# Kernel tuning notes

Hardware: AMD Instinct MI355X
Metric: run time of the kernel (lower is better)

Reference implementation:

```python
import jax, jax.numpy as jnp
import numpy as np

N_HEAD = 16

def setup_inputs() -> dict:
    key = jax.random.key(0)
    ks = jax.random.split(key, 5)
    B, S, C = 4, 2048, 1024
    x = jax.random.normal(ks[0], (B, S, C), dtype=jnp.float32)
    w_qkv = jax.random.normal(ks[1], (C, 3 * C), dtype=jnp.float32) * (1.0 / np.sqrt(C))
    b_qkv = jnp.zeros((3 * C,), dtype=jnp.float32)
    w_proj = jax.random.normal(ks[2], (C, C), dtype=jnp.float32) * (1.0 / np.sqrt(C))
    b_proj = jnp.zeros((C,), dtype=jnp.float32)
    return {"x": x, "w_qkv": w_qkv, "b_qkv": b_qkv, "w_proj": w_proj, "b_proj": b_proj}

def reference(x, w_qkv, b_qkv, w_proj, b_proj):
    B, S, C = x.shape
    H = N_HEAD
    D = C // H
    qkv = x @ w_qkv + b_qkv                       # [B,S,3C]
    q, k, v = jnp.split(qkv, 3, axis=-1)
    # [B,S,C] -> [B,H,S,D]
    q = q.reshape(B, S, H, D).transpose(0, 2, 1, 3)
    k = k.reshape(B, S, H, D).transpose(0, 2, 1, 3)
    v = v.reshape(B, S, H, D).transpose(0, 2, 1, 3)
    scores = jnp.einsum('bhqd,bhkd->bhqk', q, k) / jnp.sqrt(jnp.float32(D))
    causal = jnp.tril(jnp.ones((S, S), dtype=bool))
    scores = jnp.where(causal[None, None], scores, -jnp.inf)
    weights = jax.nn.softmax(scores, axis=-1)     # dropout p=0 -> identity
    out = jnp.einsum('bhqk,bhkd->bhqd', weights, v)
    out = out.transpose(0, 2, 1, 3).reshape(B, S, C)
    return out @ w_proj + b_proj
```

## Files before the change

### kernel.cpp

```cpp
#include <hip/hip_runtime.h>

#define SDIM 2048
#define CDIM 1024
#define BDIM 4
#define HDIM 16
#define DDIM 64

#define ATT_SCALE 0.18033688011112042f

typedef __attribute__((ext_vector_type(8))) short bf16x8;
typedef __attribute__((ext_vector_type(4))) short bf16x4;
typedef __attribute__((ext_vector_type(4))) float f32x4;
typedef unsigned short u16;

#define MFMA __builtin_amdgcn_mfma_f32_16x16x32_bf16
#define LDS_ORDER_FENCE() __asm__ __volatile__("" ::: "memory")

__device__ __forceinline__ u16 f2b(float f) {
    union { float f; unsigned u; } v; v.f = f;
    unsigned r = v.u + 0x7FFFu + ((v.u >> 16) & 1u);
    return (u16)(r >> 16);
}
__device__ __forceinline__ u16 f2b_trunc(float f) {
    union { float f; unsigned u; } v; v.f = f;
    return (u16)(v.u >> 16);
}

typedef const __attribute__((address_space(1))) unsigned int* gas_t;
typedef __attribute__((address_space(3))) unsigned int* las_t;
__device__ __forceinline__ void cp16(const void* g, void* l) {
    __builtin_amdgcn_global_load_lds((gas_t)g, (las_t)l, 16, 0, 0);
}

__device__ __forceinline__ float fast_exp2(float x) {
#if __has_builtin(__builtin_amdgcn_exp2f)
    return __builtin_amdgcn_exp2f(x);
#else
    return __exp2f(x);
#endif
}

__global__ __launch_bounds__(256) void prep(
    const float* __restrict__ x, const float* __restrict__ w_qkv,
    const float* __restrict__ w_proj,
    u16* __restrict__ Xb, u16* __restrict__ WqT, u16* __restrict__ WpT)
{
    __shared__ __align__(16) u16 t[64][72];
    const int bx = blockIdx.x;
    const int tid = threadIdx.x;

    if (bx < 4096) {
        int i = (bx * 256 + tid) * 8;
        float4 a = *reinterpret_cast<const float4*>(&x[i]);
        float4 b = *reinterpret_cast<const float4*>(&x[i + 4]);
        u16 u[8];
        u[0]=f2b(a.x); u[1]=f2b(a.y); u[2]=f2b(a.z); u[3]=f2b(a.w);
        u[4]=f2b(b.x); u[5]=f2b(b.y); u[6]=f2b(b.z); u[7]=f2b(b.w);
        *reinterpret_cast<uint4*>(&Xb[i]) = *reinterpret_cast<uint4*>(u);
        return;
    }

    const float* src; u16* dst; int N, n0, k0;
    if (bx < 4096 + 768) {
        int b2 = bx - 4096;
        src = w_qkv; dst = WqT; N = 3 * CDIM;
        n0 = (b2 % 48) * 64; k0 = (b2 / 48) * 64;
    } else {
        int b2 = bx - 4864;
        src = w_proj; dst = WpT; N = CDIM;
        n0 = (b2 % 16) * 64; k0 = (b2 / 16) * 64;
    }
    const int K = CDIM;
#pragma unroll
    for (int it = 0; it < 4; it++) {
        int c = tid + it * 256;
        int r = c >> 4, c4 = (c & 15) * 4;
        float4 f = *reinterpret_cast<const float4*>(&src[(size_t)(k0 + r) * N + n0 + c4]);
        t[c4 + 0][r] = f2b(f.x);
        t[c4 + 1][r] = f2b(f.y);
        t[c4 + 2][r] = f2b(f.z);
        t[c4 + 3][r] = f2b(f.w);
    }
    __syncthreads();
#pragma unroll
    for (int it = 0; it < 2; it++) {
        int c = tid + it * 256;
        int r = c >> 3, c8 = (c & 7) * 8;
        *reinterpret_cast<uint4*>(&dst[(size_t)(n0 + r) * K + k0 + c8]) =
            *reinterpret_cast<const uint4*>(&t[r][c8]);
    }
}

#define PHASE_TAIL()                                                          \
    LDS_ORDER_FENCE();                                                        \
    __builtin_amdgcn_s_barrier();                                             \
    __asm__ __volatile__("s_waitcnt lgkmcnt(0)" ::: "memory");                \
    __builtin_amdgcn_sched_barrier(0)

#define PHASE_END()                                                           \
    LDS_ORDER_FENCE();                                                        \
    __builtin_amdgcn_s_barrier()

__global__ __launch_bounds__(256, 2) void gemm_qkv(
    const u16* __restrict__ A, const u16* __restrict__ Bt,
    const float* __restrict__ bias,
    u16* __restrict__ Qb, u16* __restrict__ Kb, u16* __restrict__ Vtb)
{
    __shared__ __align__(16) u16 smem[3 * 8192 + 3 * 4096];
    u16* const AsAll = smem;
    u16* const BsAll = smem + 3 * 8192;

    const int tid = threadIdx.x, lane = tid & 63, wave = tid >> 6;
    const int wm = wave >> 1, wn = wave & 1;
    const int l16 = lane & 15, quad = lane >> 4;
    const int bid = blockIdx.x;
    const int w = (bid & 7) * 96 + (bid >> 3);
    const int bx = w % 24, by = w / 24;
    const int m0 = by * 256, n0 = bx * 128;
    const int K = CDIM;

    const int su = (tid & 7) ^ ((tid >> 3) & 7);
    const int sr = ((tid >> 3) << 1) | (su >> 2);
    const int sc = su & 3;

    const int uc8 = ((((l16 & 1) << 2) | quad) ^ (l16 >> 1)) * 8;
    const int faB = (wm * 64 + (l16 >> 1)) * 64 + uc8;
    const int fbB = (wn * 32 + (l16 >> 1)) * 64 + uc8;

#define STG_A(sb, k0, s)  cp16(&A [(size_t)(m0 + (s) * 64 + sr) * K + (k0) + sc * 8], \
                               &AsAll[(sb) * 8192 + ((s) * 256 + wave * 64) * 8])
#define STG_B(sb, k0, s)  cp16(&Bt[(size_t)(n0 + (s) * 64 + sr) * K + (k0) + sc * 8], \
                               &BsAll[(sb) * 4096 + ((s) * 256 + wave * 64) * 8])
#define FRA(i) (*reinterpret_cast<const bf16x8*>(&AsB[faB + (i) * 512]))
#define FRB(j) (*reinterpret_cast<const bf16x8*>(&BsB[fbB + (j) * 512]))

    f32x4 acc[8][4];
#pragma unroll
    for (int i = 0; i < 8; i++)
#pragma unroll
        for (int j = 0; j < 4; j++) acc[i][j] = (f32x4){0.f, 0.f, 0.f, 0.f};

    const int NT = K / 32;
    STG_A(0, 0, 0); STG_A(0, 0, 1); STG_A(0, 0, 2); STG_A(0, 0, 3);
    STG_B(0, 0, 0); STG_B(0, 0, 1);
    STG_A(1, 32, 0); STG_A(1, 32, 1); STG_A(1, 32, 2); STG_A(1, 32, 3);
    STG_B(1, 32, 0); STG_B(1, 32, 1);
    __asm__ __volatile__("s_waitcnt vmcnt(6)" ::: "memory");
    __builtin_amdgcn_s_barrier();
    LDS_ORDER_FENCE();

    for (int t = 0; t < NT; t++) {
        const int buf = t % 3, sbuf = (t + 2) % 3;
        const int kst = (t + 2) * 32;
        const bool st = (t + 2) < NT;
        const u16* AsB = &AsAll[buf * 8192];
        const u16* BsB = &BsAll[buf * 4096];

        bf16x8 b0, b1, b2, b3, a0, a1, a2, a3;

        b0 = FRB(0); b1 = FRB(1); b2 = FRB(2); b3 = FRB(3);
        a0 = FRA(0); a1 = FRA(1); a2 = FRA(2); a3 = FRA(3);
        if (st) { STG_A(sbuf, kst, 0); STG_A(sbuf, kst, 1); STG_A(sbuf, kst, 2); }
        PHASE_TAIL();
        __builtin_amdgcn_s_setprio(1);
        acc[0][0] = MFMA(a0, b0, acc[0][0], 0, 0, 0);
        acc[0][1] = MFMA(a0, b1, acc[0][1], 0, 0, 0);
        acc[0][2] = MFMA(a0, b2, acc[0][2], 0, 0, 0);
        acc[0][3] = MFMA(a0, b3, acc[0][3], 0, 0, 0);
        acc[1][0] = MFMA(a1, b0, acc[1][0], 0, 0, 0);
        acc[1][1] = MFMA(a1, b1, acc[1][1], 0, 0, 0);
        acc[1][2] = MFMA(a1, b2, acc[1][2], 0, 0, 0);
        acc[1][3] = MFMA(a1, b3, acc[1][3], 0, 0, 0);
        acc[2][0] = MFMA(a2, b0, acc[2][0], 0, 0, 0);
        acc[2][1] = MFMA(a2, b1, acc[2][1], 0, 0, 0);
        acc[2][2] = MFMA(a2, b2, acc[2][2], 0, 0, 0);
        acc[2][3] = MFMA(a2, b3, acc[2][3], 0, 0, 0);
        acc[3][0] = MFMA(a3, b0, acc[3][0], 0, 0, 0);
        acc[3][1] = MFMA(a3, b1, acc[3][1], 0, 0, 0);
        acc[3][2] = MFMA(a3, b2, acc[3][2], 0, 0, 0);
        acc[3][3] = MFMA(a3, b3, acc[3][3], 0, 0, 0);
        __builtin_amdgcn_s_setprio(0);
        PHASE_END();

        a0 = FRA(4); a1 = FRA(5); a2 = FRA(6); a3 = FRA(7);
        if (st) { STG_A(sbuf, kst, 3); STG_B(sbuf, kst, 0); STG_B(sbuf, kst, 1); }
        PHASE_TAIL();
        __builtin_amdgcn_s_setprio(1);
        acc[4][0] = MFMA(a0, b0, acc[4][0], 0, 0, 0);
        acc[4][1] = MFMA(a0, b1, acc[4][1], 0, 0, 0);
        acc[4][2] = MFMA(a0, b2, acc[4][2], 0, 0, 0);
        acc[4][3] = MFMA(a0, b3, acc[4][3], 0, 0, 0);
        acc[5][0] = MFMA(a1, b0, acc[5][0], 0, 0, 0);
        acc[5][1] = MFMA(a1, b1, acc[5][1], 0, 0, 0);
        acc[5][2] = MFMA(a1, b2, acc[5][2], 0, 0, 0);
        acc[5][3] = MFMA(a1, b3, acc[5][3], 0, 0, 0);
        acc[6][0] = MFMA(a2, b0, acc[6][0], 0, 0, 0);
        acc[6][1] = MFMA(a2, b1, acc[6][1], 0, 0, 0);
        acc[6][2] = MFMA(a2, b2, acc[6][2], 0, 0, 0);
        acc[6][3] = MFMA(a2, b3, acc[6][3], 0, 0, 0);
        acc[7][0] = MFMA(a3, b0, acc[7][0], 0, 0, 0);
        acc[7][1] = MFMA(a3, b1, acc[7][1], 0, 0, 0);
        acc[7][2] = MFMA(a3, b2, acc[7][2], 0, 0, 0);
        acc[7][3] = MFMA(a3, b3, acc[7][3], 0, 0, 0);
        __builtin_amdgcn_s_setprio(0);
        if (t < NT - 2) {
            __asm__ __volatile__("s_waitcnt vmcnt(6)" ::: "memory");
        } else if (t == NT - 2) {
            __asm__ __volatile__("s_waitcnt vmcnt(0)" ::: "memory");
        }
        PHASE_END();
    }
#undef STG_A
#undef STG_B
#undef FRA
#undef FRB

    const int mm0 = m0 + wm * 128;
    const int bidx = mm0 >> 11, s0 = mm0 & 2047;
    const int n_base = n0 + wn * 64;
    u16* eb = &smem[wave * (16 * 68)];
    const int erow = lane >> 2, ec = (lane & 3) * 16;

    if (n0 >= 2 * CDIM) {
        const int h = (n_base - 2 * CDIM) >> 6;
        const size_t gb = ((size_t)(bidx * HDIM + h)) * DDIM * SDIM;
#pragma unroll
        for (int ih = 0; ih < 2; ih++) {
#pragma unroll
            for (int j = 0; j < 4; j++) {
                float bvj = bias[n_base + j * 16 + l16];
                LDS_ORDER_FENCE();
#pragma unroll
                for (int i = 0; i < 4; i++)
#pragma unroll
                    for (int r = 0; r < 4; r++)
                        eb[l16 * 68 + i * 16 + quad * 4 + r] =
                            f2b(acc[ih * 4 + i][j][r] + bvj);
                LDS_ORDER_FENCE();
                union { bf16x4 hp[4]; uint4 u[2]; } pk;
                pk.hp[0] = *reinterpret_cast<const bf16x4*>(&eb[erow * 68 + ec]);
                pk.hp[1] = *reinterpret_cast<const bf16x4*>(&eb[erow * 68 + ec + 4]);
                pk.hp[2] = *reinterpret_cast<const bf16x4*>(&eb[erow * 68 + ec + 8]);
                pk.hp[3] = *reinterpret_cast<const bf16x4*>(&eb[erow * 68 + ec + 12]);
                u16* gp = &Vtb[gb + (size_t)(j * 16 + erow) * SDIM + s0 + ih * 64 + ec];
                *reinterpret_cast<uint4*>(gp)     = pk.u[0];
                *reinterpret_cast<uint4*>(gp + 8) = pk.u[1];
            }
        }
    } else {
        const bool isK = (n_base >= CDIM);
        u16* dst = isK ? Kb : Qb;
        const float scale = isK ? 1.0f : ATT_SCALE;
        const int hh = (n_base & 1023) >> 6;
        const size_t hb = ((size_t)(bidx * HDIM + hh)) * SDIM;
        float bvj[4];
#pragma unroll
        for (int j = 0; j < 4; j++) bvj[j] = bias[n_base + j * 16 + l16];
#pragma unroll
        for (int i = 0; i < 8; i++) {
            LDS_ORDER_FENCE();
#pragma unroll
            for (int j = 0; j < 4; j++)
#pragma unroll
                for (int r = 0; r < 4; r++)
                    eb[(quad * 4 + r) * 68 + j * 16 + l16] =
                        f2b((acc[i][j][r] + bvj[j]) * scale);
            LDS_ORDER_FENCE();
            union { bf16x4 hp[4]; uint4 u[2]; } pk;
            pk.hp[0] = *reinterpret_cast<const bf16x4*>(&eb[erow * 68 + ec]);
            pk.hp[1] = *reinterpret_cast<const bf16x4*>(&eb[erow * 68 + ec + 4]);
            pk.hp[2] = *reinterpret_cast<const bf16x4*>(&eb[erow * 68 + ec + 8]);
            pk.hp[3] = *reinterpret_cast<const bf16x4*>(&eb[erow * 68 + ec + 12]);
            const int s = s0 + i * 16 + erow;
            u16* gp = &dst[(hb + s) * DDIM + ec];
            *reinterpret_cast<uint4*>(gp)     = pk.u[0];
            *reinterpret_cast<uint4*>(gp + 8) = pk.u[1];
        }
    }
}

__global__ __launch_bounds__(512, 4) void attn(
    const u16* __restrict__ Qb, const u16* __restrict__ Kb,
    const u16* __restrict__ Vtb, u16* __restrict__ Ob)
{
    __shared__ __align__(16) u16 Ks[2][64 * 64];
    __shared__ __align__(16) u16 Vts[2][64 * 64];
    __shared__ __align__(16) u16 Ps[8][32 * 68];

    const int tid = threadIdx.x;
    const int lane = tid & 63, wave = tid >> 6;
    const int l16 = lane & 15, quad = lane >> 4;
    const int x = blockIdx.x;
    const int bh = (x & 7) * 8 + ((x >> 3) & 7);
    const int g8 = (x >> 6) & 3;
    const int qt = (x >> 8) ? g8 : (7 - g8);
    const int q0 = qt * 256;
    const int b = bh >> 4, h = bh & 15;
    const size_t base = (size_t)bh * (SDIM * DDIM);

    const int cl0 = wave * 64 + lane;
    const int sr0 = cl0 >> 3, scc = cl0 & 7;
    const int sg0 = scc ^ (sr0 & 7);

    const int qr0 = q0 + wave * 32 + l16;
    bf16x8 aq0 = *reinterpret_cast<const bf16x8*>(&Qb[base + (size_t)qr0 * DDIM + quad * 8]);
    bf16x8 aq1 = *reinterpret_cast<const bf16x8*>(&Qb[base + (size_t)qr0 * DDIM + 32 + quad * 8]);
    const int qr1 = qr0 + 16;
    bf16x8 aq2 = *reinterpret_cast<const bf16x8*>(&Qb[base + (size_t)qr1 * DDIM + quad * 8]);
    bf16x8 aq3 = *reinterpret_cast<const bf16x8*>(&Qb[base + (size_t)qr1 * DDIM + 32 + quad * 8]);

    u16* Pw = &Ps[wave][0];

    f32x4 O[2][4];
    f32x4 Osum[2];
#pragma unroll
    for (int g = 0; g < 2; g++) {
        Osum[g] = (f32x4){0.f, 0.f, 0.f, 0.f};
#pragma unroll
        for (int j = 0; j < 4; j++) O[g][j] = (f32x4){0.f, 0.f, 0.f, 0.f};
    }
    const short onev = (l16 == 0) ? (short)0x3F80 : (short)0;
    const bf16x8 bones = {onev, onev, onev, onev, onev, onev, onev, onev};

    const int nkb = (qt + 1) * 4;
    const int Arow = q0 + wave * 32;

    cp16(&Kb [base + (size_t)sr0 * DDIM + sg0 * 8], &Ks[0][wave * 512]);
    cp16(&Vtb[base + (size_t)sr0 * SDIM + sg0 * 8], &Vts[0][wave * 512]);

    for (int kbi = 0; kbi < nkb; kbi++) {
        const int cur = kbi & 1;
        const int kb = kbi * 64;
        __syncthreads();
        if (kbi + 1 < nkb) {
            const int kb2 = kb + 64;
            cp16(&Kb [base + (size_t)(kb2 + sr0) * DDIM + sg0 * 8], &Ks[1 - cur][wave * 512]);
            cp16(&Vtb[base + (size_t)sr0 * SDIM + kb2 + sg0 * 8], &Vts[1 - cur][wave * 512]);
        }
        if (kb > Arow + 31) continue;

        const u16* Kc = &Ks[cur][0];
        const u16* Vc = &Vts[cur][0];

        f32x4 sc0[4], sc1[4];
#pragma unroll
        for (int j = 0; j < 4; j++) {
            int kr = j * 16 + l16;
            bf16x8 bk0 = *reinterpret_cast<const bf16x8*>(&Kc[(kr * 8 + ( quad      ^ (kr & 7))) * 8]);
            bf16x8 bk1 = *reinterpret_cast<const bf16x8*>(&Kc[(kr * 8 + ((quad + 4) ^ (kr & 7))) * 8]);
            f32x4 s = (f32x4){0.f, 0.f, 0.f, 0.f};
            s = MFMA(aq0, bk0, s, 0, 0, 0);
            s = MFMA(aq1, bk1, s, 0, 0, 0);
            sc0[j] = s;
            s = (f32x4){0.f, 0.f, 0.f, 0.f};
            s = MFMA(aq2, bk0, s, 0, 0, 0);
            s = MFMA(aq3, bk1, s, 0, 0, 0);
            sc1[j] = s;
        }
        if (kb + 63 > Arow) {
            const int qrel0 = Arow - kb;
#pragma unroll
            for (int j = 0; j < 4; j++) {
                int kk = j * 16 + l16;
#pragma unroll
                for (int r = 0; r < 4; r++) {
                    sc0[j][r] = (kk <= qrel0 + quad * 4 + r)      ? sc0[j][r] : -1e30f;
                    sc1[j][r] = (kk <= qrel0 + 16 + quad * 4 + r) ? sc1[j][r] : -1e30f;
                }
            }
        }
#pragma unroll
        for (int j = 0; j < 4; j++)
#pragma unroll
            for (int r = 0; r < 4; r++) {
                Pw[(quad * 4 + r) * 68 + j * 16 + l16]        = f2b_trunc(fast_exp2(sc0[j][r]));
                Pw[(16 + quad * 4 + r) * 68 + j * 16 + l16]   = f2b_trunc(fast_exp2(sc1[j][r]));
            }
        LDS_ORDER_FENCE();
        union { bf16x4 hp[2]; bf16x8 f; } a0u, a1u, a2u, a3u;
        a0u.hp[0] = *reinterpret_cast<const bf16x4*>(&Pw[l16 * 68 + quad * 8]);
        a0u.hp[1] = *reinterpret_cast<const bf16x4*>(&Pw[l16 * 68 + quad * 8 + 4]);
        a1u.hp[0] = *reinterpret_cast<const bf16x4*>(&Pw[l16 * 68 + 32 + quad * 8]);
        a1u.hp[1] = *reinterpret_cast<const bf16x4*>(&Pw[l16 * 68 + 32 + quad * 8 + 4]);
        a2u.hp[0] = *reinterpret_cast<const bf16x4*>(&Pw[(16 + l16) * 68 + quad * 8]);
        a2u.hp[1] = *reinterpret_cast<const bf16x4*>(&Pw[(16 + l16) * 68 + quad * 8 + 4]);
        a3u.hp[0] = *reinterpret_cast<const bf16x4*>(&Pw[(16 + l16) * 68 + 32 + quad * 8]);
        a3u.hp[1] = *reinterpret_cast<const bf16x4*>(&Pw[(16 + l16) * 68 + 32 + quad * 8 + 4]);

#pragma unroll
        for (int j = 0; j < 4; j++) {
            int vr = j * 16 + l16;
            bf16x8 bv0 = *reinterpret_cast<const bf16x8*>(&Vc[(vr * 8 + ( quad      ^ (vr & 7))) * 8]);
            bf16x8 bv1 = *reinterpret_cast<const bf16x8*>(&Vc[(vr * 8 + ((quad + 4) ^ (vr & 7))) * 8]);
            O[0][j] = MFMA(a0u.f, bv0, O[0][j], 0, 0, 0);
            O[0][j] = MFMA(a1u.f, bv1, O[0][j], 0, 0, 0);
            O[1][j] = MFMA(a2u.f, bv0, O[1][j], 0, 0, 0);
            O[1][j] = MFMA(a3u.f, bv1, O[1][j], 0, 0, 0);
        }
        Osum[0] = MFMA(a0u.f, bones, Osum[0], 0, 0, 0);
        Osum[0] = MFMA(a1u.f, bones, Osum[0], 0, 0, 0);
        Osum[1] = MFMA(a2u.f, bones, Osum[1], 0, 0, 0);
        Osum[1] = MFMA(a3u.f, bones, Osum[1], 0, 0, 0);
    }

#pragma unroll
    for (int g = 0; g < 2; g++) {
#pragma unroll
        for (int r = 0; r < 4; r++) {
            float l = __shfl(Osum[g][r], (lane & 48));
            float inv = 1.0f / l;
            int s = q0 + wave * 32 + g * 16 + quad * 4 + r;
#pragma unroll
            for (int j = 0; j < 4; j++)
                Ob[((size_t)(b * SDIM + s)) * CDIM + h * 64 + j * 16 + l16] =
                    f2b(O[g][j][r] * inv);
        }
    }
}

__global__ __launch_bounds__(512, 2) void gemm_proj(
    const u16* __restrict__ A, const u16* __restrict__ Bt,
    const float* __restrict__ bias, float* __restrict__ out)
{
    __shared__ __align__(16) u16 smem[3 * 16384 + 3 * 8192];
    u16* const AsAll = smem;
    u16* const BsAll = smem + 3 * 16384;

    const int tid = threadIdx.x, lane = tid & 63, wave = tid >> 6;
    const int wm = wave >> 1, wn = wave & 1;
    const int l16 = lane & 15, quad = lane >> 4;
    const int bid = blockIdx.x;
    const int w = (bid & 7) * 32 + (bid >> 3);
    const int bx = w & 7, by = w >> 3;
    const int m0 = by * 256, n0 = bx * 128;
    const int K = CDIM, N = CDIM;

    const int l8 = lane & 7, lr = lane >> 3;
    const int sg = l8 ^ lr;
    const int arow = wave * 8 + lr;

#define STG_A(sb, k0, s)  cp16(&A [(size_t)(m0 + (s) * 64 + arow) * K + (k0) + sg * 8], \
                               &AsAll[(sb) * 16384 + ((s) * 512 + wave * 64) * 8])
#define STG_B(sb, k0, s)  cp16(&Bt[(size_t)(n0 + (s) * 64 + arow) * K + (k0) + sg * 8], \
                               &BsAll[(sb) * 8192 + ((s) * 512 + wave * 64) * 8])
#define FRA(i, kk) (*reinterpret_cast<const bf16x8*>(                                   \
        &AsB[((wm * 64 + (i) * 16 + l16) * 8 + (((kk) * 4 + quad) ^ (l16 & 7))) * 8]))
#define FRB(j, kk) (*reinterpret_cast<const bf16x8*>(                                   \
        &BsB[((wn * 64 + (j) * 16 + l16) * 8 + (((kk) * 4 + quad) ^ (l16 & 7))) * 8]))

    f32x4 acc[4][4];
#pragma unroll
    for (int i = 0; i < 4; i++)
#pragma unroll
        for (int j = 0; j < 4; j++) acc[i][j] = (f32x4){0.f, 0.f, 0.f, 0.f};

    const int NT = K / 64;
    STG_A(0, 0, 0); STG_A(0, 0, 1); STG_A(0, 0, 2); STG_A(0, 0, 3);
    STG_B(0, 0, 0); STG_B(0, 0, 1);
    STG_A(1, 64, 0); STG_A(1, 64, 1); STG_A(1, 64, 2); STG_A(1, 64, 3);
    STG_B(1, 64, 0); STG_B(1, 64, 1);
    __asm__ __volatile__("s_waitcnt vmcnt(6)" ::: "memory");
    __builtin_amdgcn_s_barrier();
    LDS_ORDER_FENCE();

    for (int t = 0; t < NT; t++) {
        const int buf = t % 3, sbuf = (t + 2) % 3;
        const int kst = (t + 2) * 64;
        const bool st = (t + 2) < NT;
        const u16* AsB = &AsAll[buf * 16384];
        const u16* BsB = &BsAll[buf * 8192];

        bf16x8 b0, b1, b2, b3, a0, a1;

        b0 = FRB(0, 0); b1 = FRB(1, 0); b2 = FRB(2, 0); b3 = FRB(3, 0);
        a0 = FRA(0, 0); a1 = FRA(1, 0);
        if (st) { STG_A(sbuf, kst, 0); STG_A(sbuf, kst, 1); }
        PHASE_TAIL();
        __builtin_amdgcn_s_setprio(1);
        acc[0][0] = MFMA(a0, b0, acc[0][0], 0, 0, 0);
        acc[0][1] = MFMA(a0, b1, acc[0][1], 0, 0, 0);
        acc[0][2] = MFMA(a0, b2, acc[0][2], 0, 0, 0);
        acc[0][3] = MFMA(a0, b3, acc[0][3], 0, 0, 0);
        acc[1][0] = MFMA(a1, b0, acc[1][0], 0, 0, 0);
        acc[1][1] = MFMA(a1, b1, acc[1][1], 0, 0, 0);
        acc[1][2] = MFMA(a1, b2, acc[1][2], 0, 0, 0);
        acc[1][3] = MFMA(a1, b3, acc[1][3], 0, 0, 0);
        __builtin_amdgcn_s_setprio(0);
        PHASE_END();

        a0 = FRA(2, 0); a1 = FRA(3, 0);
        if (st) { STG_A(sbuf, kst, 2); STG_A(sbuf, kst, 3); }
        PHASE_TAIL();
        __builtin_amdgcn_s_setprio(1);
        acc[2][0] = MFMA(a0, b0, acc[2][0], 0, 0, 0);
        acc[2][1] = MFMA(a0, b1, acc[2][1], 0, 0, 0);
        acc[2][2] = MFMA(a0, b2, acc[2][2], 0, 0, 0);
        acc[2][3] = MFMA(a0, b3, acc[2][3], 0, 0, 0);
        acc[3][0] = MFMA(a1, b0, acc[3][0], 0, 0, 0);
        acc[3][1] = MFMA(a1, b1, acc[3][1], 0, 0, 0);
        acc[3][2] = MFMA(a1, b2, acc[3][2], 0, 0, 0);
        acc[3][3] = MFMA(a1, b3, acc[3][3], 0, 0, 0);
        __builtin_amdgcn_s_setprio(0);
        PHASE_END();

        b0 = FRB(0, 1); b1 = FRB(1, 1); b2 = FRB(2, 1); b3 = FRB(3, 1);
        a0 = FRA(0, 1); a1 = FRA(1, 1);
        if (st) { STG_B(sbuf, kst, 0); STG_B(sbuf, kst, 1); }
        PHASE_TAIL();
        __builtin_amdgcn_s_setprio(1);
        acc[0][0] = MFMA(a0, b0, acc[0][0], 0, 0, 0);
        acc[0][1] = MFMA(a0, b1, acc[0][1], 0, 0, 0);
        acc[0][2] = MFMA(a0, b2, acc[0][2], 0, 0, 0);
        acc[0][3] = MFMA(a0, b3, acc[0][3], 0, 0, 0);
        acc[1][0] = MFMA(a1, b0, acc[1][0], 0, 0, 0);
        acc[1][1] = MFMA(a1, b1, acc[1][1], 0, 0, 0);
        acc[1][2] = MFMA(a1, b2, acc[1][2], 0, 0, 0);
        acc[1][3] = MFMA(a1, b3, acc[1][3], 0, 0, 0);
        __builtin_amdgcn_s_setprio(0);
        PHASE_END();

        a0 = FRA(2, 1); a1 = FRA(3, 1);
        PHASE_TAIL();
        __builtin_amdgcn_s_setprio(1);
        acc[2][0] = MFMA(a0, b0, acc[2][0], 0, 0, 0);
        acc[2][1] = MFMA(a0, b1, acc[2][1], 0, 0, 0);
        acc[2][2] = MFMA(a0, b2, acc[2][2], 0, 0, 0);
        acc[2][3] = MFMA(a0, b3, acc[2][3], 0, 0, 0);
        acc[3][0] = MFMA(a1, b0, acc[3][0], 0, 0, 0);
        acc[3][1] = MFMA(a1, b1, acc[3][1], 0, 0, 0);
        acc[3][2] = MFMA(a1, b2, acc[3][2], 0, 0, 0);
        acc[3][3] = MFMA(a1, b3, acc[3][3], 0, 0, 0);
        __builtin_amdgcn_s_setprio(0);
        if (t < NT - 2) {
            __asm__ __volatile__("s_waitcnt vmcnt(6)" ::: "memory");
        } else if (t == NT - 2) {
            __asm__ __volatile__("s_waitcnt vmcnt(0)" ::: "memory");
        }
        PHASE_END();
    }
#undef STG_A
#undef STG_B
#undef FRA
#undef FRB

#pragma unroll
    for (int i = 0; i < 4; i++) {
        int mbase = m0 + wm * 64 + i * 16 + quad * 4;
#pragma unroll
        for (int j = 0; j < 4; j++) {
            int n = n0 + wn * 64 + j * 16 + l16;
            float bv = bias[n];
#pragma unroll
            for (int r = 0; r < 4; r++)
                out[(size_t)(mbase + r) * N + n] = acc[i][j][r] + bv;
        }
    }
}

extern "C" void kernel_launch(void* const* d_in, const int* in_sizes, int n_in,
                              void* d_out, int out_size, void* d_ws, size_t ws_size,
                              hipStream_t stream) {
    const float* x      = (const float*)d_in[0];
    const float* w_qkv  = (const float*)d_in[1];
    const float* b_qkv  = (const float*)d_in[2];
    const float* w_proj = (const float*)d_in[3];
    const float* b_proj = (const float*)d_in[4];
    float* out = (float*)d_out;

    const size_t per = (size_t)BDIM * HDIM * SDIM * DDIM;
    u16* Qb  = (u16*)d_ws;
    u16* Kb  = Qb + per;
    u16* Vtb = Kb + per;
    u16* Ob  = Vtb + per;
    u16* Xb  = Ob;
    u16* WqT = Ob + per;
    u16* WpT = WqT + (size_t)3 * CDIM * CDIM;

    prep<<<dim3(4096 + 768 + 256), dim3(256), 0, stream>>>(x, w_qkv, w_proj, Xb, WqT, WpT);

    gemm_qkv<<<dim3(768), dim3(256), 0, stream>>>(Xb, WqT, b_qkv, Qb, Kb, Vtb);
    attn<<<dim3(512), dim3(512), 0, stream>>>(Qb, Kb, Vtb, Ob);
    gemm_proj<<<dim3(256), dim3(512), 0, stream>>>(Ob, WpT, b_proj, out);
}
```

Baseline: 234.1 us.

## Simplify GEMM main loops to one barrier per tile and rework proj tiling

The qkv GEMM loop drops its two-phase schedule, which used per-phase barriers, explicit lgkmcnt waits, sched_barriers and setprio. It now loads all fragments, issues every async copy, then runs all 32 MFMAs with a single barrier per K-tile, leaving the interleaving to the compiler. The proj GEMM is rebuilt to match the qkv kernel: 256 threads, 8x4 accumulators per wave, BK=32 and the same swizzled staging layout, in place of the 512-thread BK=64 version. Fewer barriers cut synchronisation overhead, at the risk of weaker overlap between LDS reads, global loads and MFMA issue, plus higher register pressure.

```diff
diff --git a/kernel.cpp b/kernel.cpp
--- a/kernel.cpp
+++ b/kernel.cpp
@@ -15,6 +15,11 @@
 
 #define MFMA __builtin_amdgcn_mfma_f32_16x16x32_bf16
 #define LDS_ORDER_FENCE() __asm__ __volatile__("" ::: "memory")
+
+#define TILE_BAR()                                                            \
+    LDS_ORDER_FENCE();                                                        \
+    __builtin_amdgcn_s_barrier();                                             \
+    LDS_ORDER_FENCE()
 
 __device__ __forceinline__ u16 f2b(float f) {
     union { float f; unsigned u; } v; v.f = f;
@@ -91,16 +96,6 @@
     }
 }
 
-#define PHASE_TAIL()                                                          \
-    LDS_ORDER_FENCE();                                                        \
-    __builtin_amdgcn_s_barrier();                                             \
-    __asm__ __volatile__("s_waitcnt lgkmcnt(0)" ::: "memory");                \
-    __builtin_amdgcn_sched_barrier(0)
-
-#define PHASE_END()                                                           \
-    LDS_ORDER_FENCE();                                                        \
-    __builtin_amdgcn_s_barrier()
-
 __global__ __launch_bounds__(256, 2) void gemm_qkv(
     const u16* __restrict__ A, const u16* __restrict__ Bt,
     const float* __restrict__ bias,
@@ -146,8 +141,7 @@
     STG_A(1, 32, 0); STG_A(1, 32, 1); STG_A(1, 32, 2); STG_A(1, 32, 3);
     STG_B(1, 32, 0); STG_B(1, 32, 1);
     __asm__ __volatile__("s_waitcnt vmcnt(6)" ::: "memory");
-    __builtin_amdgcn_s_barrier();
-    LDS_ORDER_FENCE();
+    TILE_BAR();
 
     for (int t = 0; t < NT; t++) {
         const int buf = t % 3, sbuf = (t + 2) % 3;
@@ -156,59 +150,28 @@
         const u16* AsB = &AsAll[buf * 8192];
         const u16* BsB = &BsAll[buf * 4096];
 
-        bf16x8 b0, b1, b2, b3, a0, a1, a2, a3;
-
-        b0 = FRB(0); b1 = FRB(1); b2 = FRB(2); b3 = FRB(3);
-        a0 = FRA(0); a1 = FRA(1); a2 = FRA(2); a3 = FRA(3);
-        if (st) { STG_A(sbuf, kst, 0); STG_A(sbuf, kst, 1); STG_A(sbuf, kst, 2); }
-        PHASE_TAIL();
-        __builtin_amdgcn_s_setprio(1);
-        acc[0][0] = MFMA(a0, b0, acc[0][0], 0, 0, 0);
-        acc[0][1] = MFMA(a0, b1, acc[0][1], 0, 0, 0);
-        acc[0][2] = MFMA(a0, b2, acc[0][2], 0, 0, 0);
-        acc[0][3] = MFMA(a0, b3, acc[0][3], 0, 0, 0);
-        acc[1][0] = MFMA(a1, b0, acc[1][0], 0, 0, 0);
-        acc[1][1] = MFMA(a1, b1, acc[1][1], 0, 0, 0);
-        acc[1][2] = MFMA(a1, b2, acc[1][2], 0, 0, 0);
-        acc[1][3] = MFMA(a1, b3, acc[1][3], 0, 0, 0);
-        acc[2][0] = MFMA(a2, b0, acc[2][0], 0, 0, 0);
-        acc[2][1] = MFMA(a2, b1, acc[2][1], 0, 0, 0);
-        acc[2][2] = MFMA(a2, b2, acc[2][2], 0, 0, 0);
-        acc[2][3] = MFMA(a2, b3, acc[2][3], 0, 0, 0);
-        acc[3][0] = MFMA(a3, b0, acc[3][0], 0, 0, 0);
-        acc[3][1] = MFMA(a3, b1, acc[3][1], 0, 0, 0);
-        acc[3][2] = MFMA(a3, b2, acc[3][2], 0, 0, 0);
-        acc[3][3] = MFMA(a3, b3, acc[3][3], 0, 0, 0);
-        __builtin_amdgcn_s_setprio(0);
-        PHASE_END();
-
-        a0 = FRA(4); a1 = FRA(5); a2 = FRA(6); a3 = FRA(7);
-        if (st) { STG_A(sbuf, kst, 3); STG_B(sbuf, kst, 0); STG_B(sbuf, kst, 1); }
-        PHASE_TAIL();
-        __builtin_amdgcn_s_setprio(1);
-        acc[4][0] = MFMA(a0, b0, acc[4][0], 0, 0, 0);
-        acc[4][1] = MFMA(a0, b1, acc[4][1], 0, 0, 0);
-        acc[4][2] = MFMA(a0, b2, acc[4][2], 0, 0, 0);
-        acc[4][3] = MFMA(a0, b3, acc[4][3], 0, 0, 0);
-        acc[5][0] = MFMA(a1, b0, acc[5][0], 0, 0, 0);
-        acc[5][1] = MFMA(a1, b1, acc[5][1], 0, 0, 0);
-        acc[5][2] = MFMA(a1, b2, acc[5][2], 0, 0, 0);
-        acc[5][3] = MFMA(a1, b3, acc[5][3], 0, 0, 0);
-        acc[6][0] = MFMA(a2, b0, acc[6][0], 0, 0, 0);
-        acc[6][1] = MFMA(a2, b1, acc[6][1], 0, 0, 0);
-        acc[6][2] = MFMA(a2, b2, acc[6][2], 0, 0, 0);
-        acc[6][3] = MFMA(a2, b3, acc[6][3], 0, 0, 0);
-        acc[7][0] = MFMA(a3, b0, acc[7][0], 0, 0, 0);
-        acc[7][1] = MFMA(a3, b1, acc[7][1], 0, 0, 0);
-        acc[7][2] = MFMA(a3, b2, acc[7][2], 0, 0, 0);
-        acc[7][3] = MFMA(a3, b3, acc[7][3], 0, 0, 0);
-        __builtin_amdgcn_s_setprio(0);
+        bf16x8 av[8], bv[4];
+#pragma unroll
+        for (int j = 0; j < 4; j++) bv[j] = FRB(j);
+#pragma unroll
+        for (int i = 0; i < 8; i++) av[i] = FRA(i);
+        if (st) {
+            STG_A(sbuf, kst, 0); STG_A(sbuf, kst, 1);
+            STG_A(sbuf, kst, 2); STG_A(sbuf, kst, 3);
+            STG_B(sbuf, kst, 0); STG_B(sbuf, kst, 1);
+        }
+#pragma unroll
+        for (int i = 0; i < 8; i++)
+#pragma unroll
+            for (int j = 0; j < 4; j++)
+                acc[i][j] = MFMA(av[i], bv[j], acc[i][j], 0, 0, 0);
+
         if (t < NT - 2) {
             __asm__ __volatile__("s_waitcnt vmcnt(6)" ::: "memory");
         } else if (t == NT - 2) {
             __asm__ __volatile__("s_waitcnt vmcnt(0)" ::: "memory");
         }
-        PHASE_END();
+        TILE_BAR();
     }
 #undef STG_A
 #undef STG_B
@@ -418,13 +381,13 @@
     }
 }
 
-__global__ __launch_bounds__(512, 2) void gemm_proj(
+__global__ __launch_bounds__(256, 2) void gemm_proj(
     const u16* __restrict__ A, const u16* __restrict__ Bt,
     const float* __restrict__ bias, float* __restrict__ out)
 {
-    __shared__ __align__(16) u16 smem[3 * 16384 + 3 * 8192];
+    __shared__ __align__(16) u16 smem[3 * 8192 + 3 * 4096];
     u16* const AsAll = smem;
-    u16* const BsAll = smem + 3 * 16384;
+    u16* const BsAll = smem + 3 * 8192;
 
     const int tid = threadIdx.x, lane = tid & 63, wave = tid >> 6;
     const int wm = wave >> 1, wn = wave & 1;
@@ -435,108 +398,64 @@
     const int m0 = by * 256, n0 = bx * 128;
     const int K = CDIM, N = CDIM;
 
-    const int l8 = lane & 7, lr = lane >> 3;
-    const int sg = l8 ^ lr;
-    const int arow = wave * 8 + lr;
-
-#define STG_A(sb, k0, s)  cp16(&A [(size_t)(m0 + (s) * 64 + arow) * K + (k0) + sg * 8], \
-                               &AsAll[(sb) * 16384 + ((s) * 512 + wave * 64) * 8])
-#define STG_B(sb, k0, s)  cp16(&Bt[(size_t)(n0 + (s) * 64 + arow) * K + (k0) + sg * 8], \
-                               &BsAll[(sb) * 8192 + ((s) * 512 + wave * 64) * 8])
-#define FRA(i, kk) (*reinterpret_cast<const bf16x8*>(                                   \
-        &AsB[((wm * 64 + (i) * 16 + l16) * 8 + (((kk) * 4 + quad) ^ (l16 & 7))) * 8]))
-#define FRB(j, kk) (*reinterpret_cast<const bf16x8*>(                                   \
-        &BsB[((wn * 64 + (j) * 16 + l16) * 8 + (((kk) * 4 + quad) ^ (l16 & 7))) * 8]))
-
-    f32x4 acc[4][4];
-#pragma unroll
-    for (int i = 0; i < 4; i++)
+    const int su = (tid & 7) ^ ((tid >> 3) & 7);
+    const int sr = ((tid >> 3) << 1) | (su >> 2);
+    const int sc = su & 3;
+
+    const int uc8 = ((((l16 & 1) << 2) | quad) ^ (l16 >> 1)) * 8;
+    const int faB = (wm * 64 + (l16 >> 1)) * 64 + uc8;
+    const int fbB = (wn * 32 + (l16 >> 1)) * 64 + uc8;
+
+#define STG_A(sb, k0, s)  cp16(&A [(size_t)(m0 + (s) * 64 + sr) * K + (k0) + sc * 8], \
+                               &AsAll[(sb) * 8192 + ((s) * 256 + wave * 64) * 8])
+#define STG_B(sb, k0, s)  cp16(&Bt[(size_t)(n0 + (s) * 64 + sr) * K + (k0) + sc * 8], \
+                               &BsAll[(sb) * 4096 + ((s) * 256 + wave * 64) * 8])
+#define FRA(i) (*reinterpret_cast<const bf16x8*>(&AsB[faB + (i) * 512]))
+#define FRB(j) (*reinterpret_cast<const bf16x8*>(&BsB[fbB + (j) * 512]))
+
+    f32x4 acc[8][4];
+#pragma unroll
+    for (int i = 0; i < 8; i++)
 #pragma unroll
         for (int j = 0; j < 4; j++) acc[i][j] = (f32x4){0.f, 0.f, 0.f, 0.f};
 
-    const int NT = K / 64;
+    const int NT = K / 32;
     STG_A(0, 0, 0); STG_A(0, 0, 1); STG_A(0, 0, 2); STG_A(0, 0, 3);
     STG_B(0, 0, 0); STG_B(0, 0, 1);
-    STG_A(1, 64, 0); STG_A(1, 64, 1); STG_A(1, 64, 2); STG_A(1, 64, 3);
-    STG_B(1, 64, 0); STG_B(1, 64, 1);
+    STG_A(1, 32, 0); STG_A(1, 32, 1); STG_A(1, 32, 2); STG_A(1, 32, 3);
+    STG_B(1, 32, 0); STG_B(1, 32, 1);
     __asm__ __volatile__("s_waitcnt vmcnt(6)" ::: "memory");
-    __builtin_amdgcn_s_barrier();
-    LDS_ORDER_FENCE();
+    TILE_BAR();
 
     for (int t = 0; t < NT; t++) {
         const int buf = t % 3, sbuf = (t + 2) % 3;
-        const int kst = (t + 2) * 64;
+        const int kst = (t + 2) * 32;
         const bool st = (t + 2) < NT;
-        const u16* AsB = &AsAll[buf * 16384];
-        const u16* BsB = &BsAll[buf * 8192];
-
-        bf16x8 b0, b1, b2, b3, a0, a1;
-
-        b0 = FRB(0, 0); b1 = FRB(1, 0); b2 = FRB(2, 0); b3 = FRB(3, 0);
-        a0 = FRA(0, 0); a1 = FRA(1, 0);
-        if (st) { STG_A(sbuf, kst, 0); STG_A(sbuf, kst, 1); }
-        PHASE_TAIL();
-        __builtin_amdgcn_s_setprio(1);
-        acc[0][0] = MFMA(a0, b0, acc[0][0], 0, 0, 0);
-        acc[0][1] = MFMA(a0, b1, acc[0][1], 0, 0, 0);
-        acc[0][2] = MFMA(a0, b2, acc[0][2], 0, 0, 0);
-        acc[0][3] = MFMA(a0, b3, acc[0][3], 0, 0, 0);
-        acc[1][0] = MFMA(a1, b0, acc[1][0], 0, 0, 0);
-        acc[1][1] = MFMA(a1, b1, acc[1][1], 0, 0, 0);
-        acc[1][2] = MFMA(a1, b2, acc[1][2], 0, 0, 0);
-        acc[1][3] = MFMA(a1, b3, acc[1][3], 0, 0, 0);
-        __builtin_amdgcn_s_setprio(0);
-        PHASE_END();
-
-        a0 = FRA(2, 0); a1 = FRA(3, 0);
-        if (st) { STG_A(sbuf, kst, 2); STG_A(sbuf, kst, 3); }
-        PHASE_TAIL();
-        __builtin_amdgcn_s_setprio(1);
-        acc[2][0] = MFMA(a0, b0, acc[2][0], 0, 0, 0);
-        acc[2][1] = MFMA(a0, b1, acc[2][1], 0, 0, 0);
-        acc[2][2] = MFMA(a0, b2, acc[2][2], 0, 0, 0);
-        acc[2][3] = MFMA(a0, b3, acc[2][3], 0, 0, 0);
-        acc[3][0] = MFMA(a1, b0, acc[3][0], 0, 0, 0);
-        acc[3][1] = MFMA(a1, b1, acc[3][1], 0, 0, 0);
-        acc[3][2] = MFMA(a1, b2, acc[3][2], 0, 0, 0);
-        acc[3][3] = MFMA(a1, b3, acc[3][3], 0, 0, 0);
-        __builtin_amdgcn_s_setprio(0);
-        PHASE_END();
-
-        b0 = FRB(0, 1); b1 = FRB(1, 1); b2 = FRB(2, 1); b3 = FRB(3, 1);
-        a0 = FRA(0, 1); a1 = FRA(1, 1);
-        if (st) { STG_B(sbuf, kst, 0); STG_B(sbuf, kst, 1); }
-        PHASE_TAIL();
-        __builtin_amdgcn_s_setprio(1);
-        acc[0][0] = MFMA(a0, b0, acc[0][0], 0, 0, 0);
-        acc[0][1] = MFMA(a0, b1, acc[0][1], 0, 0, 0);
-        acc[0][2] = MFMA(a0, b2, acc[0][2], 0, 0, 0);
-        acc[0][3] = MFMA(a0, b3, acc[0][3], 0, 0, 0);
-        acc[1][0] = MFMA(a1, b0, acc[1][0], 0, 0, 0);
-        acc[1][1] = MFMA(a1, b1, acc[1][1], 0, 0, 0);
-        acc[1][2] = MFMA(a1, b2, acc[1][2], 0, 0, 0);
-        acc[1][3] = MFMA(a1, b3, acc[1][3], 0, 0, 0);
-        __builtin_amdgcn_s_setprio(0);
-        PHASE_END();
-
-        a0 = FRA(2, 1); a1 = FRA(3, 1);
-        PHASE_TAIL();
-        __builtin_amdgcn_s_setprio(1);
-        acc[2][0] = MFMA(a0, b0, acc[2][0], 0, 0, 0);
-        acc[2][1] = MFMA(a0, b1, acc[2][1], 0, 0, 0);
-        acc[2][2] = MFMA(a0, b2, acc[2][2], 0, 0, 0);
-        acc[2][3] = MFMA(a0, b3, acc[2][3], 0, 0, 0);
-        acc[3][0] = MFMA(a1, b0, acc[3][0], 0, 0, 0);
-        acc[3][1] = MFMA(a1, b1, acc[3][1], 0, 0, 0);
-        acc[3][2] = MFMA(a1, b2, acc[3][2], 0, 0, 0);
-        acc[3][3] = MFMA(a1, b3, acc[3][3], 0, 0, 0);
-        __builtin_amdgcn_s_setprio(0);
+        const u16* AsB = &AsAll[buf * 8192];
+        const u16* BsB = &BsAll[buf * 4096];
+
+        bf16x8 av[8], bv[4];
+#pragma unroll
+        for (int j = 0; j < 4; j++) bv[j] = FRB(j);
+#pragma unroll
+        for (int i = 0; i < 8; i++) av[i] = FRA(i);
+        if (st) {
+            STG_A(sbuf, kst, 0); STG_A(sbuf, kst, 1);
+            STG_A(sbuf, kst, 2); STG_A(sbuf, kst, 3);
+            STG_B(sbuf, kst, 0); STG_B(sbuf, kst, 1);
+        }
+#pragma unroll
+        for (int i = 0; i < 8; i++)
+#pragma unroll
+            for (int j = 0; j < 4; j++)
+                acc[i][j] = MFMA(av[i], bv[j], acc[i][j], 0, 0, 0);
+
         if (t < NT - 2) {
             __asm__ __volatile__("s_waitcnt vmcnt(6)" ::: "memory");
         } else if (t == NT - 2) {
             __asm__ __volatile__("s_waitcnt vmcnt(0)" ::: "memory");
         }
-        PHASE_END();
+        TILE_BAR();
     }
 #undef STG_A
 #undef STG_B
@@ -544,8 +463,8 @@
 #undef FRB
 
 #pragma unroll
-    for (int i = 0; i < 4; i++) {
-        int mbase = m0 + wm * 64 + i * 16 + quad * 4;
+    for (int i = 0; i < 8; i++) {
+        int mbase = m0 + wm * 128 + i * 16 + quad * 4;
 #pragma unroll
         for (int j = 0; j < 4; j++) {
             int n = n0 + wn * 64 + j * 16 + l16;
@@ -580,5 +499,5 @@
 
     gemm_qkv<<<dim3(768), dim3(256), 0, stream>>>(Xb, WqT, b_qkv, Qb, Kb, Vtb);
     attn<<<dim3(512), dim3(512), 0, stream>>>(Qb, Kb, Vtb, Ob);
-    gemm_proj<<<dim3(256), dim3(512), 0, stream>>>(Ob, WpT, b_proj, out);
-}
+    gemm_proj<<<dim3(256), dim3(256), 0, stream>>>(Ob, WpT, b_proj, out);
+}
```

After: 231.0 us. About the same (-1.3%).
